# Kernel tuning notes

Hardware: AMD Instinct MI355X
Metric: run time of the kernel (lower is better)

Reference implementation:

```python
import jax, jax.numpy as jnp
import numpy as np

N_HEADS = 16
DIM_HEAD = 64
ROPE_THETA = 10000.0


def _rope_tables(seq_len, dim_head, dtype):
    # [N, dim_head//2] angle tables, llama-style interleaved-pair rotation
    inv_freq = 1.0 / (ROPE_THETA ** (jnp.arange(0, dim_head, 2, dtype=jnp.float32) / dim_head))
    t = jnp.arange(seq_len, dtype=jnp.float32)
    freqs = jnp.outer(t, inv_freq)  # [N, D/2]
    return jnp.cos(freqs).astype(dtype), jnp.sin(freqs).astype(dtype)


def _apply_rope(x, cos, sin):
    # x: [B, H, N, D]; rotate interleaved pairs (x[2i], x[2i+1])
    xr = x[..., 0::2]
    xi = x[..., 1::2]
    cos = cos[None, None, :, :]
    sin = sin[None, None, :, :]
    out_r = xr * cos - xi * sin
    out_i = xr * sin + xi * cos
    return jnp.stack([out_r, out_i], axis=-1).reshape(x.shape)


def _l2norm(x, eps=1e-12):
    return x / jnp.maximum(jnp.linalg.norm(x, axis=-1, keepdims=True), eps)


def setup_inputs() -> dict:
    key = jax.random.key(0)
    ks = jax.random.split(key, 5)
    B, N, dim = 1, 4096, N_HEADS * DIM_HEAD
    q = jax.random.normal(ks[0], (B, N, dim), dtype=jnp.float32)
    k = jax.random.normal(ks[1], (B, N, dim), dtype=jnp.float32)
    v = jax.random.normal(ks[2], (B, N, dim), dtype=jnp.float32)
    qk_scale = jnp.full((1, 1, 1, DIM_HEAD), 10.0, dtype=jnp.float32)
    w_out = jax.random.normal(ks[3], (dim, dim), dtype=jnp.float32) * (dim ** -0.5)
    b_out = jnp.zeros((dim,), dtype=jnp.float32)
    return {"q": q, "k": k, "v": v, "qk_scale": qk_scale, "w_out": w_out, "b_out": b_out}


def reference(q, k, v, qk_scale, w_out, b_out):
    B, N, dim = q.shape
    H, D = N_HEADS, DIM_HEAD
    scale = D ** -0.5
    # [B, N, dim] -> [B, H, N, D]
    q = q.reshape(B, N, H, D).transpose(0, 2, 1, 3)
    k = k.reshape(B, N, H, D).transpose(0, 2, 1, 3)
    v = v.reshape(B, N, H, D).transpose(0, 2, 1, 3)
    # RoPE
    cos, sin = _rope_tables(N, D, q.dtype)
    q = _apply_rope(q, cos, sin)
    k = _apply_rope(k, cos, sin)
    # QK-norm: L2-normalize then learned scale
    q = _l2norm(q) * qk_scale
    k = _l2norm(k) * qk_scale
    # explicit attention (non-flash)
    scores = jnp.einsum('bhid,bhjd->bhij', q, k) * scale
    probs = jax.nn.softmax(scores, axis=-1)
    out = jnp.einsum('bhij,bhjd->bhid', probs, v)
    out = out.transpose(0, 2, 1, 3).reshape(B, N, dim)
    # Linear: y = x W^T + b
    return out @ w_out.T + b_out
```

## Files before the change

### kernel.cpp

```cpp
#include <hip/hip_runtime.h>
#include <hip/hip_bf16.h>

#define N_CTX 4096
#define NH    16
#define DH    64
#define DIM   1024
#define NSPLIT 2
#define KT_PER_SPLIT (N_CTX / 64 / NSPLIT)

typedef __attribute__((ext_vector_type(8))) short bf16x8;
typedef __attribute__((ext_vector_type(4))) float f32x4;

__device__ __forceinline__ ushort f2bf(float f) {
    union { float f; unsigned u; } x; x.f = f;
    unsigned r = (x.u + 0x7FFFu + ((x.u >> 16) & 1u)) >> 16;
    return (ushort)r;
}
__device__ __forceinline__ float bf2f(ushort u) {
    union { unsigned u; float f; } x; x.u = ((unsigned)u) << 16; return x.f;
}
__device__ __forceinline__ unsigned fbits(float f) {
    union { float f; unsigned u; } x; x.f = f; return x.u;
}
__device__ __forceinline__ unsigned pack_bf16(float lo, float hi) {
    unsigned a = fbits(lo) + 0x8000u;
    unsigned b = fbits(hi) + 0x8000u;
#if defined(__has_builtin)
#if __has_builtin(__builtin_amdgcn_perm)
    return __builtin_amdgcn_perm(b, a, 0x07060302u);
#else
    return (a >> 16) | (b & 0xFFFF0000u);
#endif
#else
    return (a >> 16) | (b & 0xFFFF0000u);
#endif
}
__device__ __forceinline__ float fast_exp2(float x) {
#if defined(__has_builtin)
#if __has_builtin(__builtin_amdgcn_exp2f)
    return __builtin_amdgcn_exp2f(x);
#else
    return exp2f(x);
#endif
#else
    return exp2f(x);
#endif
}
__device__ __forceinline__ void fast_sincos(float ang, float* s, float* c) {
#if defined(__has_builtin)
#if __has_builtin(__builtin_amdgcn_sinf) && __has_builtin(__builtin_amdgcn_cosf) && __has_builtin(__builtin_amdgcn_fractf)
    float rev = __builtin_amdgcn_fractf(ang * 0.15915494309189535f);
    *s = __builtin_amdgcn_sinf(rev);
    *c = __builtin_amdgcn_cosf(rev);
    return;
#endif
#endif
    sincosf(ang, s, c);
}

#define SC 0.18033688011112042f
#define LF 0.4152410118609203f

__global__ __launch_bounds__(256) void prep_kernel(
    const float* __restrict__ qg, const float* __restrict__ kg,
    const float* __restrict__ qk_scale,
    ushort* __restrict__ qb, ushort* __restrict__ kb)
{
    const int lane = threadIdx.x & 63;
    const int wave = threadIdx.x >> 6;
    const int row  = blockIdx.x * 4 + wave;
    const int n = row >> 4;
    const int h = row & 15;
    const int isk = blockIdx.y;
    const float* __restrict__ x = isk ? kg : qg;
    ushort* __restrict__ xb = isk ? kb : qb;
    const float premul = isk ? 1.0f : SC;

    float val = x[(size_t)n * DIM + h * DH + lane];
    float other = __shfl_xor(val, 1, 64);

    const int i = lane >> 1;
    float inv_freq = fast_exp2((float)i * -LF);
    float ang = (float)n * inv_freq;
    float s, c;
    fast_sincos(ang, &s, &c);

    float r = (lane & 1) ? fmaf(other, s, val * c)
                         : fmaf(val, c, -(other * s));

    float ss = r * r;
    #pragma unroll
    for (int off = 32; off > 0; off >>= 1)
        ss += __shfl_xor(ss, off, 64);
    float invn = rsqrtf(fmaxf(ss, 1e-24f));
    float scl  = qk_scale[lane] * premul;

    xb[((size_t)h * N_CTX + n) * DH + lane] = f2bf(r * invn * scl);
}

__global__ __launch_bounds__(256) void vtrans_kernel(
    const float* __restrict__ v, ushort* __restrict__ vt)
{
    __shared__ ushort L[64][68];
    const int kt = blockIdx.x, h = blockIdx.y, t = threadIdx.x;

    for (int e = t; e < 4096; e += 256) {
        int key = e >> 6, d = e & 63;
        float f = v[(size_t)(kt * 64 + key) * DIM + h * DH + d];
        L[d][key] = f2bf(f);
    }
    __syncthreads();
    for (int e = t; e < 4096; e += 256) {
        int d = e >> 6, key = e & 63;
        vt[((size_t)h * DH + d) * N_CTX + kt * 64 + key] = L[d][key];
    }
}

__global__ __launch_bounds__(256) void wconv_kernel(
    const float* __restrict__ w, ushort* __restrict__ wb)
{
    int i = (blockIdx.x * 256 + threadIdx.x) * 4;
    float4 f = *(const float4*)&w[i];
    ushort4 u;
    u.x = f2bf(f.x); u.y = f2bf(f.y); u.z = f2bf(f.z); u.w = f2bf(f.w);
    *(ushort4*)&wb[i] = u;
}

__global__ __launch_bounds__(256) void attn_kernel(
    const ushort* __restrict__ qb, const ushort* __restrict__ kb,
    const ushort* __restrict__ vt, ushort* __restrict__ opart,
    float* __restrict__ lpart)
{
    __shared__ ushort Ks[64][72];
    __shared__ ushort Vt[64][72];
    __shared__ ushort Ps[128][72];

    const int h     = blockIdx.y;
    const int qbase = blockIdx.x * 128;
    const int sp    = blockIdx.z;
    const int kbase = sp * (N_CTX / NSPLIT);
    const int t    = threadIdx.x;
    const int w    = t >> 6;
    const int lane = t & 63;
    const int l15  = lane & 15;
    const int quad = lane >> 4;

    bf16x8 qf[2][2];
    #pragma unroll
    for (int qt = 0; qt < 2; qt++) {
        const size_t qrow = ((size_t)h * N_CTX + qbase + w * 32 + qt * 16 + l15) * DH;
        qf[qt][0] = *(const bf16x8*)&qb[qrow + quad * 8];
        qf[qt][1] = *(const bf16x8*)&qb[qrow + 32 + quad * 8];
    }

    float l_part[2] = {0.0f, 0.0f};
    f32x4 o_acc[4][2];
    #pragma unroll
    for (int dt = 0; dt < 4; dt++)
        #pragma unroll
        for (int qt = 0; qt < 2; qt++)
            o_acc[dt][qt] = (f32x4){0.f, 0.f, 0.f, 0.f};

    const int sr = t >> 3;
    const int sc = (t & 7) * 8;
    const ushort* kp0 = &kb[((size_t)h * N_CTX + kbase + sr) * DH + sc];
    const ushort* kp1 = kp0 + (size_t)32 * DH;
    const ushort* vp0 = &vt[((size_t)h * DH + sr) * N_CTX + kbase + sc];
    const ushort* vp1 = vp0 + (size_t)32 * N_CTX;
    bf16x8 kr0 = *(const bf16x8*)kp0, kr1 = *(const bf16x8*)kp1;
    bf16x8 vr0 = *(const bf16x8*)vp0, vr1 = *(const bf16x8*)vp1;

    for (int kt = 0; kt < KT_PER_SPLIT; kt++) {
        __syncthreads();
        *(bf16x8*)&Ks[sr][sc]      = kr0;
        *(bf16x8*)&Ks[sr + 32][sc] = kr1;
        *(bf16x8*)&Vt[sr][sc]      = vr0;
        *(bf16x8*)&Vt[sr + 32][sc] = vr1;
        __syncthreads();
        if (kt + 1 < KT_PER_SPLIT) {
            kr0 = *(const bf16x8*)(kp0 + (size_t)(kt + 1) * 64 * DH);
            kr1 = *(const bf16x8*)(kp1 + (size_t)(kt + 1) * 64 * DH);
            vr0 = *(const bf16x8*)(vp0 + (size_t)(kt + 1) * 64);
            vr1 = *(const bf16x8*)(vp1 + (size_t)(kt + 1) * 64);
        }

        #pragma unroll
        for (int j = 0; j < 4; j++) {
            bf16x8 kf0 = *(const bf16x8*)&Ks[j * 16 + l15][quad * 8];
            bf16x8 kf1 = *(const bf16x8*)&Ks[j * 16 + l15][32 + quad * 8];
            f32x4 s0 = (f32x4){0.f, 0.f, 0.f, 0.f};
            f32x4 s1 = (f32x4){0.f, 0.f, 0.f, 0.f};
            s0 = __builtin_amdgcn_mfma_f32_16x16x32_bf16(kf0, qf[0][0], s0, 0, 0, 0);
            s1 = __builtin_amdgcn_mfma_f32_16x16x32_bf16(kf0, qf[1][0], s1, 0, 0, 0);
            s0 = __builtin_amdgcn_mfma_f32_16x16x32_bf16(kf1, qf[0][1], s0, 0, 0, 0);
            s1 = __builtin_amdgcn_mfma_f32_16x16x32_bf16(kf1, qf[1][1], s1, 0, 0, 0);

            {
                float p0 = fast_exp2(s0.x), p1 = fast_exp2(s0.y);
                float p2 = fast_exp2(s0.z), p3 = fast_exp2(s0.w);
                l_part[0] += (p0 + p1) + (p2 + p3);
                uint2 pk; pk.x = pack_bf16(p0, p1); pk.y = pack_bf16(p2, p3);
                *(uint2*)&Ps[w * 32 + l15][j * 16 + quad * 4] = pk;
            }
            {
                float p0 = fast_exp2(s1.x), p1 = fast_exp2(s1.y);
                float p2 = fast_exp2(s1.z), p3 = fast_exp2(s1.w);
                l_part[1] += (p0 + p1) + (p2 + p3);
                uint2 pk; pk.x = pack_bf16(p0, p1); pk.y = pack_bf16(p2, p3);
                *(uint2*)&Ps[w * 32 + 16 + l15][j * 16 + quad * 4] = pk;
            }
        }

        #pragma unroll
        for (int ks = 0; ks < 2; ks++) {
            bf16x8 pf0 = *(const bf16x8*)&Ps[w * 32 + l15][ks * 32 + quad * 8];
            bf16x8 pf1 = *(const bf16x8*)&Ps[w * 32 + 16 + l15][ks * 32 + quad * 8];
            #pragma unroll
            for (int dt = 0; dt < 4; dt++) {
                bf16x8 vf = *(const bf16x8*)&Vt[dt * 16 + l15][ks * 32 + quad * 8];
                o_acc[dt][0] = __builtin_amdgcn_mfma_f32_16x16x32_bf16(vf, pf0, o_acc[dt][0], 0, 0, 0);
                o_acc[dt][1] = __builtin_amdgcn_mfma_f32_16x16x32_bf16(vf, pf1, o_acc[dt][1], 0, 0, 0);
            }
        }
    }

    #pragma unroll
    for (int qt = 0; qt < 2; qt++) {
        float v = l_part[qt];
        v += __shfl_xor(v, 16, 64);
        v += __shfl_xor(v, 32, 64);
        if (quad == 0)
            lpart[(size_t)sp * NH * N_CTX + (size_t)h * N_CTX
                  + qbase + w * 32 + qt * 16 + l15] = v;
    }

    #pragma unroll
    for (int qt = 0; qt < 2; qt++)
        #pragma unroll
        for (int dt = 0; dt < 4; dt++) {
            f32x4 o = o_acc[dt][qt];
            ushort4 ov;
            ov.x = f2bf(o.x); ov.y = f2bf(o.y);
            ov.z = f2bf(o.z); ov.w = f2bf(o.w);
            *(ushort4*)&opart[((size_t)sp * N_CTX + qbase + w * 32 + qt * 16 + l15) * DIM
                              + h * DH + dt * 16 + quad * 4] = ov;
        }
}

__global__ __launch_bounds__(256) void combine_kernel(
    const ushort* __restrict__ opart, const float* __restrict__ lpart,
    ushort* __restrict__ attnb)
{
    const int idx = blockIdx.x * 256 + threadIdx.x;
    const int n   = idx >> 8;
    const int rem = idx & 255;
    const int h   = rem >> 4;
    const size_t e = (size_t)n * DIM + h * DH + (rem & 15) * 4;

    float s0 = 0.f, s1 = 0.f, s2 = 0.f, s3 = 0.f, lsum = 0.f;
    #pragma unroll
    for (int sp = 0; sp < NSPLIT; sp++) {
        ushort4 u = *(const ushort4*)&opart[(size_t)sp * N_CTX * DIM + e];
        s0 += bf2f(u.x); s1 += bf2f(u.y); s2 += bf2f(u.z); s3 += bf2f(u.w);
        lsum += lpart[(size_t)sp * NH * N_CTX + (size_t)h * N_CTX + n];
    }
    float li = 1.0f / lsum;

    ushort4 r;
    r.x = f2bf(s0 * li); r.y = f2bf(s1 * li);
    r.z = f2bf(s2 * li); r.w = f2bf(s3 * li);
    *(ushort4*)&attnb[e] = r;
}

__global__ __launch_bounds__(256) void proj_kernel(
    const ushort* __restrict__ A, const ushort* __restrict__ W,
    const float* __restrict__ bias, float* __restrict__ out)
{
    __shared__ ushort As[64][72];
    __shared__ ushort Ws[64][72];

    const int nbase = blockIdx.x * 64;
    const int obase = blockIdx.y * 64;
    const int t    = threadIdx.x;
    const int w    = t >> 6;
    const int lane = t & 63;
    const int l15  = lane & 15;
    const int quad = lane >> 4;
    const int rw   = (w >> 1) * 32;
    const int cw   = (w & 1) * 32;

    f32x4 acc[2][2];
    #pragma unroll
    for (int mt = 0; mt < 2; mt++)
        #pragma unroll
        for (int nt = 0; nt < 2; nt++)
            acc[mt][nt] = (f32x4){0.f, 0.f, 0.f, 0.f};

    for (int kt = 0; kt < DIM / 64; kt++) {
        const int kb = kt * 64;
        __syncthreads();
        #pragma unroll
        for (int i = 0; i < 2; i++) {
            int c = t + i * 256, r = c >> 3, c8 = c & 7;
            *(bf16x8*)&As[r][c8 * 8] =
                *(const bf16x8*)&A[(size_t)(nbase + r) * DIM + kb + c8 * 8];
        }
        #pragma unroll
        for (int i = 0; i < 2; i++) {
            int c = t + i * 256, r = c >> 3, c8 = c & 7;
            *(bf16x8*)&Ws[r][c8 * 8] =
                *(const bf16x8*)&W[(size_t)(obase + r) * DIM + kb + c8 * 8];
        }
        __syncthreads();

        bf16x8 af[2][2], bfr[2][2];
        #pragma unroll
        for (int mt = 0; mt < 2; mt++)
            #pragma unroll
            for (int kh = 0; kh < 2; kh++)
                af[mt][kh] = *(const bf16x8*)&As[rw + mt * 16 + l15][kh * 32 + quad * 8];
        #pragma unroll
        for (int nt = 0; nt < 2; nt++)
            #pragma unroll
            for (int kh = 0; kh < 2; kh++)
                bfr[nt][kh] = *(const bf16x8*)&Ws[cw + nt * 16 + l15][kh * 32 + quad * 8];

        #pragma unroll
        for (int mt = 0; mt < 2; mt++)
            #pragma unroll
            for (int nt = 0; nt < 2; nt++) {
                acc[mt][nt] = __builtin_amdgcn_mfma_f32_16x16x32_bf16(af[mt][0], bfr[nt][0], acc[mt][nt], 0, 0, 0);
                acc[mt][nt] = __builtin_amdgcn_mfma_f32_16x16x32_bf16(af[mt][1], bfr[nt][1], acc[mt][nt], 0, 0, 0);
            }
    }

    #pragma unroll
    for (int nt = 0; nt < 2; nt++) {
        int o = obase + cw + nt * 16 + l15;
        float bb = bias[o];
        #pragma unroll
        for (int mt = 0; mt < 2; mt++) {
            int nrow = nbase + rw + mt * 16 + quad * 4;
            out[(size_t)(nrow + 0) * DIM + o] = acc[mt][nt].x + bb;
            out[(size_t)(nrow + 1) * DIM + o] = acc[mt][nt].y + bb;
            out[(size_t)(nrow + 2) * DIM + o] = acc[mt][nt].z + bb;
            out[(size_t)(nrow + 3) * DIM + o] = acc[mt][nt].w + bb;
        }
    }
}

extern "C" void kernel_launch(void* const* d_in, const int* in_sizes, int n_in,
                              void* d_out, int out_size, void* d_ws, size_t ws_size,
                              hipStream_t stream)
{
    const float* q        = (const float*)d_in[0];
    const float* k        = (const float*)d_in[1];
    const float* v        = (const float*)d_in[2];
    const float* qk_scale = (const float*)d_in[3];
    const float* w_out    = (const float*)d_in[4];
    const float* b_out    = (const float*)d_in[5];
    float* out = (float*)d_out;

    const size_t per = (size_t)NH * N_CTX * DH;
    ushort* qb    = (ushort*)d_ws;
    ushort* kb    = qb + per;
    ushort* vtg   = kb + per;
    ushort* attnb = vtg + per;
    ushort* wb    = attnb + per;
    ushort* opart = wb + (size_t)DIM * DIM;
    float*  lpart = (float*)(opart + (size_t)NSPLIT * N_CTX * DIM);

    prep_kernel<<<dim3(N_CTX * NH / 4, 2), 256, 0, stream>>>(q, k, qk_scale, qb, kb);
    vtrans_kernel<<<dim3(N_CTX / 64, NH), 256, 0, stream>>>(v, vtg);
    wconv_kernel<<<dim3(DIM * DIM / 1024), 256, 0, stream>>>(w_out, wb);
    attn_kernel<<<dim3(N_CTX / 128, NH, NSPLIT), 256, 0, stream>>>(qb, kb, vtg, opart, lpart);
    combine_kernel<<<dim3(N_CTX * DIM / 4 / 256), 256, 0, stream>>>(opart, lpart, attnb);
    proj_kernel<<<dim3(N_CTX / 64, DIM / 64), 256, 0, stream>>>(attnb, wb, b_out, out);
}
```

Before: 236.5 us.

## Keep softmax probabilities in registers and feed PV via 16x16x16 MFMA

The exp'd score tile from the QK MFMA is now packed straight into a bf16x4 register operand and consumed by 16x16x16 bf16 MFMAs, instead of going through a Ps shared-memory buffer with a round trip. This removes the LDS writes, reads and the shared allocation for P, which frees LDS for occupancy. The KV split count rises from 2 to 4 and launch bounds ask for 6 blocks per CU to raise parallelism. In exchange it uses half-K MFMAs (twice as many instructions for PV) and more partial outputs to merge.

```diff
diff --git a/kernel.cpp b/kernel.cpp
--- a/kernel.cpp
+++ b/kernel.cpp
@@ -5,10 +5,11 @@
 #define NH    16
 #define DH    64
 #define DIM   1024
-#define NSPLIT 2
+#define NSPLIT 4
 #define KT_PER_SPLIT (N_CTX / 64 / NSPLIT)
 
 typedef __attribute__((ext_vector_type(8))) short bf16x8;
+typedef __attribute__((ext_vector_type(4))) short bf16x4;
 typedef __attribute__((ext_vector_type(4))) float f32x4;
 
 __device__ __forceinline__ ushort f2bf(float f) {
@@ -56,6 +57,20 @@
 #endif
 #endif
     sincosf(ang, s, c);
+}
+
+__device__ __forceinline__ f32x4 mfma16_bf16(bf16x4 a, bf16x4 b, f32x4 c) {
+#if defined(__has_builtin)
+#if __has_builtin(__builtin_amdgcn_mfma_f32_16x16x16bf16_1k)
+    return __builtin_amdgcn_mfma_f32_16x16x16bf16_1k(a, b, c, 0, 0, 0);
+#else
+    asm("v_mfma_f32_16x16x16_bf16 %0, %1, %2, %0" : "+v"(c) : "v"(a), "v"(b));
+    return c;
+#endif
+#else
+    asm("v_mfma_f32_16x16x16_bf16 %0, %1, %2, %0" : "+v"(c) : "v"(a), "v"(b));
+    return c;
+#endif
 }
 
 #define SC 0.18033688011112042f
@@ -126,14 +141,13 @@
     *(ushort4*)&wb[i] = u;
 }
 
-__global__ __launch_bounds__(256) void attn_kernel(
+__global__ __launch_bounds__(256, 6) void attn_kernel(
     const ushort* __restrict__ qb, const ushort* __restrict__ kb,
     const ushort* __restrict__ vt, ushort* __restrict__ opart,
     float* __restrict__ lpart)
 {
     __shared__ ushort Ks[64][72];
     __shared__ ushort Vt[64][72];
-    __shared__ ushort Ps[128][72];
 
     const int h     = blockIdx.y;
     const int qbase = blockIdx.x * 128;
@@ -195,31 +209,27 @@
             s0 = __builtin_amdgcn_mfma_f32_16x16x32_bf16(kf1, qf[0][1], s0, 0, 0, 0);
             s1 = __builtin_amdgcn_mfma_f32_16x16x32_bf16(kf1, qf[1][1], s1, 0, 0, 0);
 
+            bf16x4 pf0, pf1;
             {
                 float p0 = fast_exp2(s0.x), p1 = fast_exp2(s0.y);
                 float p2 = fast_exp2(s0.z), p3 = fast_exp2(s0.w);
                 l_part[0] += (p0 + p1) + (p2 + p3);
                 uint2 pk; pk.x = pack_bf16(p0, p1); pk.y = pack_bf16(p2, p3);
-                *(uint2*)&Ps[w * 32 + l15][j * 16 + quad * 4] = pk;
+                pf0 = __builtin_bit_cast(bf16x4, pk);
             }
             {
                 float p0 = fast_exp2(s1.x), p1 = fast_exp2(s1.y);
                 float p2 = fast_exp2(s1.z), p3 = fast_exp2(s1.w);
                 l_part[1] += (p0 + p1) + (p2 + p3);
                 uint2 pk; pk.x = pack_bf16(p0, p1); pk.y = pack_bf16(p2, p3);
-                *(uint2*)&Ps[w * 32 + 16 + l15][j * 16 + quad * 4] = pk;
+                pf1 = __builtin_bit_cast(bf16x4, pk);
             }
-        }
-
-        #pragma unroll
-        for (int ks = 0; ks < 2; ks++) {
-            bf16x8 pf0 = *(const bf16x8*)&Ps[w * 32 + l15][ks * 32 + quad * 8];
-            bf16x8 pf1 = *(const bf16x8*)&Ps[w * 32 + 16 + l15][ks * 32 + quad * 8];
+
             #pragma unroll
             for (int dt = 0; dt < 4; dt++) {
-                bf16x8 vf = *(const bf16x8*)&Vt[dt * 16 + l15][ks * 32 + quad * 8];
-                o_acc[dt][0] = __builtin_amdgcn_mfma_f32_16x16x32_bf16(vf, pf0, o_acc[dt][0], 0, 0, 0);
-                o_acc[dt][1] = __builtin_amdgcn_mfma_f32_16x16x32_bf16(vf, pf1, o_acc[dt][1], 0, 0, 0);
+                bf16x4 vf = *(const bf16x4*)&Vt[dt * 16 + l15][j * 16 + quad * 4];
+                o_acc[dt][0] = mfma16_bf16(vf, pf0, o_acc[dt][0]);
+                o_acc[dt][1] = mfma16_bf16(vf, pf1, o_acc[dt][1]);
             }
         }
     }
```

Result: slower. 602.3 us (+154.7%).

## Keep softmax probabilities in registers via permlane swaps; raise key split to 4

Applied to the files above, without the earlier changes.

Stops staging the exponentiated score tile P through a shared-memory buffer. It rearranges the MFMA output fragments directly into the operand layout the PV MFMA expects, using permlane32/permlane16 swap instructions (with shuffle fallbacks). This removes LDS writes and reads plus the LDS footprint for P, which may raise occupancy. It also doubles the key-dimension split to 4, adding more blocks but more partial-output traffic for the combine step.

```diff
diff --git a/kernel.cpp b/kernel.cpp
--- a/kernel.cpp
+++ b/kernel.cpp
@@ -5,11 +5,12 @@
 #define NH    16
 #define DH    64
 #define DIM   1024
-#define NSPLIT 2
+#define NSPLIT 4
 #define KT_PER_SPLIT (N_CTX / 64 / NSPLIT)
 
 typedef __attribute__((ext_vector_type(8))) short bf16x8;
 typedef __attribute__((ext_vector_type(4))) float f32x4;
+typedef __attribute__((ext_vector_type(2))) unsigned u32x2;
 
 __device__ __forceinline__ ushort f2bf(float f) {
     union { float f; unsigned u; } x; x.f = f;
@@ -56,6 +57,37 @@
 #endif
 #endif
     sincosf(ang, s, c);
+}
+
+__device__ __forceinline__ void pl32_swap(unsigned &a, unsigned &b) {
+#if defined(__has_builtin)
+#if __has_builtin(__builtin_amdgcn_permlane32_swap)
+    u32x2 r = __builtin_amdgcn_permlane32_swap(a, b, false, false);
+    a = r[0]; b = r[1];
+    return;
+#endif
+#endif
+    const int lane = (int)(threadIdx.x & 63);
+    unsigned ax = (unsigned)__shfl_xor((int)a, 32, 64);
+    unsigned bx = (unsigned)__shfl_xor((int)b, 32, 64);
+    unsigned na = (lane & 32) ? bx : a;
+    unsigned nb = (lane & 32) ? b  : ax;
+    a = na; b = nb;
+}
+__device__ __forceinline__ void pl16_swap(unsigned &a, unsigned &b) {
+#if defined(__has_builtin)
+#if __has_builtin(__builtin_amdgcn_permlane16_swap)
+    u32x2 r = __builtin_amdgcn_permlane16_swap(a, b, false, false);
+    a = r[0]; b = r[1];
+    return;
+#endif
+#endif
+    const int lane = (int)(threadIdx.x & 63);
+    unsigned ax = (unsigned)__shfl_xor((int)a, 16, 64);
+    unsigned bx = (unsigned)__shfl_xor((int)b, 16, 64);
+    unsigned na = (lane & 16) ? bx : a;
+    unsigned nb = (lane & 16) ? b  : ax;
+    a = na; b = nb;
 }
 
 #define SC 0.18033688011112042f
@@ -133,7 +165,6 @@
 {
     __shared__ ushort Ks[64][72];
     __shared__ ushort Vt[64][72];
-    __shared__ ushort Ps[128][72];
 
     const int h     = blockIdx.y;
     const int qbase = blockIdx.x * 128;
@@ -185,41 +216,56 @@
         }
 
         #pragma unroll
-        for (int j = 0; j < 4; j++) {
-            bf16x8 kf0 = *(const bf16x8*)&Ks[j * 16 + l15][quad * 8];
-            bf16x8 kf1 = *(const bf16x8*)&Ks[j * 16 + l15][32 + quad * 8];
-            f32x4 s0 = (f32x4){0.f, 0.f, 0.f, 0.f};
-            f32x4 s1 = (f32x4){0.f, 0.f, 0.f, 0.f};
-            s0 = __builtin_amdgcn_mfma_f32_16x16x32_bf16(kf0, qf[0][0], s0, 0, 0, 0);
-            s1 = __builtin_amdgcn_mfma_f32_16x16x32_bf16(kf0, qf[1][0], s1, 0, 0, 0);
-            s0 = __builtin_amdgcn_mfma_f32_16x16x32_bf16(kf1, qf[0][1], s0, 0, 0, 0);
-            s1 = __builtin_amdgcn_mfma_f32_16x16x32_bf16(kf1, qf[1][1], s1, 0, 0, 0);
-
-            {
-                float p0 = fast_exp2(s0.x), p1 = fast_exp2(s0.y);
-                float p2 = fast_exp2(s0.z), p3 = fast_exp2(s0.w);
-                l_part[0] += (p0 + p1) + (p2 + p3);
-                uint2 pk; pk.x = pack_bf16(p0, p1); pk.y = pack_bf16(p2, p3);
-                *(uint2*)&Ps[w * 32 + l15][j * 16 + quad * 4] = pk;
+        for (int jp = 0; jp < 2; jp++) {
+            unsigned pa[2][2], pb[2][2];
+            #pragma unroll
+            for (int jj = 0; jj < 2; jj++) {
+                const int j = jp * 2 + jj;
+                bf16x8 kf0 = *(const bf16x8*)&Ks[j * 16 + l15][quad * 8];
+                bf16x8 kf1 = *(const bf16x8*)&Ks[j * 16 + l15][32 + quad * 8];
+                f32x4 s0 = (f32x4){0.f, 0.f, 0.f, 0.f};
+                f32x4 s1 = (f32x4){0.f, 0.f, 0.f, 0.f};
+                s0 = __builtin_amdgcn_mfma_f32_16x16x32_bf16(kf0, qf[0][0], s0, 0, 0, 0);
+                s1 = __builtin_amdgcn_mfma_f32_16x16x32_bf16(kf0, qf[1][0], s1, 0, 0, 0);
+                s0 = __builtin_amdgcn_mfma_f32_16x16x32_bf16(kf1, qf[0][1], s0, 0, 0, 0);
+                s1 = __builtin_amdgcn_mfma_f32_16x16x32_bf16(kf1, qf[1][1], s1, 0, 0, 0);
+
+                {
+                    float p0 = fast_exp2(s0.x), p1 = fast_exp2(s0.y);
+                    float p2 = fast_exp2(s0.z), p3 = fast_exp2(s0.w);
+                    l_part[0] += (p0 + p1) + (p2 + p3);
+                    unsigned d0 = pack_bf16(p0, p1), d1 = pack_bf16(p2, p3);
+                    if (jj == 0) { pa[0][0] = d0; pa[0][1] = d1; }
+                    else         { pb[0][0] = d0; pb[0][1] = d1; }
+                }
+                {
+                    float p0 = fast_exp2(s1.x), p1 = fast_exp2(s1.y);
+                    float p2 = fast_exp2(s1.z), p3 = fast_exp2(s1.w);
+                    l_part[1] += (p0 + p1) + (p2 + p3);
+                    unsigned d0 = pack_bf16(p0, p1), d1 = pack_bf16(p2, p3);
+                    if (jj == 0) { pa[1][0] = d0; pa[1][1] = d1; }
+                    else         { pb[1][0] = d0; pb[1][1] = d1; }
+                }
             }
-            {
-                float p0 = fast_exp2(s1.x), p1 = fast_exp2(s1.y);
-                float p2 = fast_exp2(s1.z), p3 = fast_exp2(s1.w);
-                l_part[1] += (p0 + p1) + (p2 + p3);
-                uint2 pk; pk.x = pack_bf16(p0, p1); pk.y = pack_bf16(p2, p3);
-                *(uint2*)&Ps[w * 32 + 16 + l15][j * 16 + quad * 4] = pk;
+
+            bf16x8 pw[2];
+            #pragma unroll
+            for (int qt = 0; qt < 2; qt++) {
+                unsigned x0 = pa[qt][0], y0 = pb[qt][0];
+                unsigned x1 = pa[qt][1], y1 = pb[qt][1];
+                pl32_swap(x0, y0);
+                pl32_swap(x1, y1);
+                pl16_swap(x0, y0);
+                pl16_swap(x1, y1);
+                uint4 wd; wd.x = x0; wd.y = x1; wd.z = y0; wd.w = y1;
+                pw[qt] = __builtin_bit_cast(bf16x8, wd);
             }
-        }
-
-        #pragma unroll
-        for (int ks = 0; ks < 2; ks++) {
-            bf16x8 pf0 = *(const bf16x8*)&Ps[w * 32 + l15][ks * 32 + quad * 8];
-            bf16x8 pf1 = *(const bf16x8*)&Ps[w * 32 + 16 + l15][ks * 32 + quad * 8];
+
             #pragma unroll
             for (int dt = 0; dt < 4; dt++) {
-                bf16x8 vf = *(const bf16x8*)&Vt[dt * 16 + l15][ks * 32 + quad * 8];
-                o_acc[dt][0] = __builtin_amdgcn_mfma_f32_16x16x32_bf16(vf, pf0, o_acc[dt][0], 0, 0, 0);
-                o_acc[dt][1] = __builtin_amdgcn_mfma_f32_16x16x32_bf16(vf, pf1, o_acc[dt][1], 0, 0, 0);
+                bf16x8 vf = *(const bf16x8*)&Vt[dt * 16 + l15][jp * 32 + quad * 8];
+                o_acc[dt][0] = __builtin_amdgcn_mfma_f32_16x16x32_bf16(vf, pw[0], o_acc[dt][0], 0, 0, 0);
+                o_acc[dt][1] = __builtin_amdgcn_mfma_f32_16x16x32_bf16(vf, pw[1], o_acc[dt][1], 0, 0, 0);
             }
         }
     }
```

Result: no change. 240.0 us (+1.5%).
